# Kernel optimization log

Hardware: AMD Instinct MI355X
Metric: run time of the kernel (lower is better)

Reference implementation:

```python
import jax, jax.numpy as jnp
import numpy as np

B, T, C = 2, 2048, 2048
NH, NKVH = 16, 4
HS = C // NH          # 128
KV = NKVH * HS        # 512
ROPE_BASE = 10000.0


def setup_inputs() -> dict:
    key = jax.random.key(0)
    k0, k1, k2 = jax.random.split(key, 3)
    x = jax.random.normal(k0, (B, T, C), dtype=jnp.float32)
    w_qkv = jax.random.normal(k1, (C, C + 2 * KV), dtype=jnp.float32) * 0.02
    b_qkv = jnp.zeros((C + 2 * KV,), dtype=jnp.float32)
    w_proj = jax.random.normal(k2, (C, C), dtype=jnp.float32) * 0.02
    b_proj = jnp.zeros((C,), dtype=jnp.float32)
    # RoPE frequencies: freqs_cis[t, j] = exp(i * t * base^(-2j/HS)), j in [0, HS/2)
    inv_freq = 1.0 / (ROPE_BASE ** (jnp.arange(0, HS, 2, dtype=jnp.float32) / HS))
    ang = jnp.arange(T, dtype=jnp.float32)[:, None] * inv_freq[None, :]  # [T, HS/2]
    return {
        "x": x, "w_qkv": w_qkv, "b_qkv": b_qkv,
        "w_proj": w_proj, "b_proj": b_proj,
        "freqs_cos": jnp.cos(ang), "freqs_sin": jnp.sin(ang),
    }


def _apply_rope(x, cos, sin):
    # x: [B, T, H, HS]; pairs (even, odd) along last dim are (real, imag)
    b, t, h, d = x.shape
    x_ = x.reshape(b, t, h, d // 2, 2)
    xr, xi = x_[..., 0], x_[..., 1]
    cos = cos[None, :, None, :]  # [1, T, 1, HS/2]
    sin = sin[None, :, None, :]
    out_r = xr * cos - xi * sin
    out_i = xr * sin + xi * cos
    return jnp.stack([out_r, out_i], axis=-1).reshape(b, t, h, d)


def reference(x, w_qkv, b_qkv, w_proj, b_proj, freqs_cos, freqs_sin):
    qkv = x @ w_qkv + b_qkv                      # [B, T, C + 2*KV]
    q, k, v = jnp.split(qkv, [C, C + KV], axis=2)
    q = q.reshape(B, T, NH, HS)
    k = k.reshape(B, T, NKVH, HS)
    v = v.reshape(B, T, NKVH, HS).transpose(0, 2, 1, 3)  # [B, NKVH, T, HS]
    q = _apply_rope(q, freqs_cos, freqs_sin)
    k = _apply_rope(k, freqs_cos, freqs_sin)
    q = q.transpose(0, 2, 1, 3)                  # [B, NH, T, HS]
    k = k.transpose(0, 2, 1, 3)                  # [B, NKVH, T, HS]
    kv_cache = (k, v)
    rep = NH // NKVH
    k_full = jnp.repeat(k, rep, axis=1)          # repeat_interleave on head dim
    v_full = jnp.repeat(v, rep, axis=1)
    scores = jnp.einsum("bhqd,bhkd->bhqk", q, k_full) / jnp.sqrt(jnp.float32(HS))
    causal = jnp.tril(jnp.ones((T, T), dtype=bool))
    scores = jnp.where(causal[None, None], scores, jnp.finfo(scores.dtype).min)
    attn = jax.nn.softmax(scores, axis=-1)
    y = jnp.einsum("bhqk,bhkd->bhqd", attn, v_full)
    y = y.transpose(0, 2, 1, 3).reshape(B, T, C)
    y = y @ w_proj + b_proj
    return y, kv_cache[0], kv_cache[1]
```

## Files before the change

kernel.cpp:

```cpp
#include <hip/hip_runtime.h>

typedef unsigned short u16;
typedef unsigned int u32;

#define B_    2
#define T_    2048
#define C_    2048
#define NH_   16
#define NKVH_ 4
#define HS_   128
#define NQKV  3072
#define M_    4096
#define SCALE 0.08838834764831845f
#define CC    0.12751742f
#define THR_RAW 62.0f

typedef __bf16 bf16x8 __attribute__((ext_vector_type(8)));
typedef float  f32x4  __attribute__((ext_vector_type(4)));
typedef float  f32x16 __attribute__((ext_vector_type(16)));
typedef unsigned int u32x2 __attribute__((ext_vector_type(2)));

__device__ __forceinline__ float bf2f(u16 u) {
    union { u32 i; float f; } x; x.i = ((u32)u) << 16; return x.f;
}
__device__ __forceinline__ u16 f2bf(float f) {
    union { float f; u32 i; } x; x.f = f;
    u32 r = x.i + 0x7fffu + ((x.i >> 16) & 1u);
    return (u16)(r >> 16);
}
__device__ __forceinline__ u32 cvtpk(float lo, float hi) {
    u32 r; asm("v_cvt_pk_bf16_f32 %0, %1, %2" : "=v"(r) : "v"(lo), "v"(hi));
    return r;
}

__device__ __forceinline__ void gload16(const void* g, void* l) {
    __builtin_amdgcn_global_load_lds(
        (const __attribute__((address_space(1))) u32*)g,
        (__attribute__((address_space(3))) u32*)l,
        16, 0, 0);
}

__global__ __launch_bounds__(256) void cast_f32_bf16(
    const float* __restrict__ in, u16* __restrict__ out, int n)
{
    int idx = (blockIdx.x * 256 + threadIdx.x) * 4;
    if (idx < n) {
        float4 v = *reinterpret_cast<const float4*>(in + idx);
        u32 p0 = (u32)f2bf(v.x) | ((u32)f2bf(v.y) << 16);
        u32 p1 = (u32)f2bf(v.z) | ((u32)f2bf(v.w) << 16);
        u32* o = (u32*)(out + idx);
        o[0] = p0; o[1] = p1;
    }
}

__global__ __launch_bounds__(256) void transpose_cast_f32_bf16(
    const float* __restrict__ in, u16* __restrict__ out, int R, int Cc)
{
    __shared__ float tile[32][33];
    int c0 = blockIdx.x * 32, r0 = blockIdx.y * 32;
    int tx = threadIdx.x & 31, ty = threadIdx.x >> 5;
#pragma unroll
    for (int i = 0; i < 4; ++i)
        tile[ty + i * 8][tx] = in[(size_t)(r0 + ty + i * 8) * Cc + c0 + tx];
    __syncthreads();
#pragma unroll
    for (int i = 0; i < 4; ++i)
        out[(size_t)(c0 + ty + i * 8) * R + r0 + tx] = f2bf(tile[tx][ty + i * 8]);
}

__global__ __launch_bounds__(256) void transpose_bf16_batched(
    const u16* __restrict__ in, u16* __restrict__ out, int R, int Cc)
{
    __shared__ u16 tile[32][33];
    int c0 = blockIdx.x * 32, r0 = blockIdx.y * 32;
    size_t zb = (size_t)blockIdx.z * R * Cc;
    int tx = threadIdx.x & 31, ty = threadIdx.x >> 5;
#pragma unroll
    for (int i = 0; i < 4; ++i)
        tile[ty + i * 8][tx] = in[zb + (size_t)(r0 + ty + i * 8) * Cc + c0 + tx];
    __syncthreads();
#pragma unroll
    for (int i = 0; i < 4; ++i)
        out[zb + (size_t)(c0 + ty + i * 8) * R + r0 + tx] = tile[tx][ty + i * 8];
}

template <int MFRAG, int OUT_BF16>
__global__ __launch_bounds__(512, 2) void gemm8(
    const u16* __restrict__ A, const u16* __restrict__ Bt,
    const float* __restrict__ bias, void* __restrict__ Cv,
    int M, int N, int K)
{
    constexpr int MH = MFRAG / 2;
    constexpr int LA = MFRAG / 4;
    constexpr int ASZ = MFRAG * 1024;
    __shared__ __attribute__((aligned(16))) u16 As[2][2][ASZ];
    __shared__ __attribute__((aligned(16))) u16 Bs[2][2][8192];

    int tid = threadIdx.x, lane = tid & 63, w = tid >> 6;
    int l16 = lane & 15, hi = (lane >> 4) & 3;
    int wm = w >> 2, wn = w & 3;

    int gx = gridDim.x, nwg = gx * gridDim.y;
    int id = blockIdx.y * gx + blockIdx.x;
    int nid = (id & 7) * (nwg >> 3) + (id >> 3);
    int brow = (nid % gx) * (MFRAG * 32), bcol = (nid / gx) * 256;

    const int NT = K >> 6;
    f32x4 acc[MFRAG][4] = {};

    auto stageA = [&](int kt2, int kk, int buf) {
#pragma unroll
        for (int i = 0; i < LA; ++i) {
            u32 off = (u32)i * 8192 + (u32)w * 1024 + ((u32)lane << 4);
            u32 g = off ^ (((off >> 7) & 7) << 4);
            u32 r = g >> 6, s = (g >> 4) & 3;
            gload16(A + (size_t)(brow + r) * K + kt2 * 64 + kk * 32 + s * 8,
                    (char*)&As[buf][kk][0] + i * 8192 + w * 1024);
        }
    };
    auto stageB = [&](int kt2, int kk, int buf) {
#pragma unroll
        for (int i = 0; i < 2; ++i) {
            u32 off = (u32)i * 8192 + (u32)w * 1024 + ((u32)lane << 4);
            u32 g = off ^ (((off >> 7) & 7) << 4);
            u32 r = g >> 6, s = (g >> 4) & 3;
            gload16(Bt + (size_t)(bcol + r) * K + kt2 * 64 + kk * 32 + s * 8,
                    (char*)&Bs[buf][kk][0] + i * 8192 + w * 1024);
        }
    };
    auto readA = [&](const u16* base, int mh, bf16x8* dst) {
#pragma unroll
        for (int m = 0; m < MH; ++m) {
            u32 a = (u32)((wm * MFRAG + mh * MH + m) * 16 + l16) * 64 + (u32)hi * 16;
            dst[m] = *reinterpret_cast<const bf16x8*>(
                (const char*)base + (a ^ (((a >> 7) & 7) << 4)));
        }
    };
    auto readB = [&](const u16* base, bf16x8* dst) {
#pragma unroll
        for (int n = 0; n < 4; ++n) {
            u32 a = (u32)(wn * 64 + n * 16 + l16) * 64 + (u32)hi * 16;
            dst[n] = *reinterpret_cast<const bf16x8*>(
                (const char*)base + (a ^ (((a >> 7) & 7) << 4)));
        }
    };

    stageA(0, 0, 0); stageB(0, 0, 0); stageA(0, 1, 0); stageB(0, 1, 0);
    if (NT > 1) {
        stageA(1, 0, 1); stageB(1, 0, 1); stageA(1, 1, 1);
        if constexpr (MFRAG == 8) asm volatile("s_waitcnt vmcnt(6)" ::: "memory");
        else                      asm volatile("s_waitcnt vmcnt(4)" ::: "memory");
    } else {
        asm volatile("s_waitcnt vmcnt(0)" ::: "memory");
    }
    __builtin_amdgcn_s_barrier();

    for (int kt = 0; kt < NT; ++kt) {
        int cur = kt & 1, nxt = cur ^ 1;
        const u16* Ac0 = &As[cur][0][0];
        const u16* Ac1 = &As[cur][1][0];
        const u16* Bc0 = &Bs[cur][0][0];
        const u16* Bc1 = &Bs[cur][1][0];
        bf16x8 af0[MH], af1[MH], af2[MH], af3[MH], bf0[4], bf1[4];

        readA(Ac0, 0, af0); readB(Bc0, bf0); readA(Ac0, 1, af1);
        if (kt + 1 < NT) stageB(kt + 1, 1, nxt);
        __builtin_amdgcn_s_barrier();
        __builtin_amdgcn_s_setprio(1);
#pragma unroll
        for (int m = 0; m < MH; ++m)
#pragma unroll
            for (int n = 0; n < 4; ++n)
                acc[m][n] = __builtin_amdgcn_mfma_f32_16x16x32_bf16(
                    af0[m], bf0[n], acc[m][n], 0, 0, 0);
        __builtin_amdgcn_s_setprio(0);
        __builtin_amdgcn_s_barrier();

        readA(Ac1, 0, af2); readB(Bc1, bf1);
        if (kt + 2 < NT) stageA(kt + 2, 0, cur);
        __builtin_amdgcn_s_barrier();
        __builtin_amdgcn_s_setprio(1);
#pragma unroll
        for (int m = 0; m < MH; ++m)
#pragma unroll
            for (int n = 0; n < 4; ++n)
                acc[MH + m][n] = __builtin_amdgcn_mfma_f32_16x16x32_bf16(
                    af1[m], bf0[n], acc[MH + m][n], 0, 0, 0);
        __builtin_amdgcn_s_setprio(0);
        __builtin_amdgcn_s_barrier();

        readA(Ac1, 1, af3);
        if (kt + 2 < NT) stageB(kt + 2, 0, cur);
        __builtin_amdgcn_s_barrier();
        __builtin_amdgcn_s_setprio(1);
#pragma unroll
        for (int m = 0; m < MH; ++m)
#pragma unroll
            for (int n = 0; n < 4; ++n)
                acc[m][n] = __builtin_amdgcn_mfma_f32_16x16x32_bf16(
                    af2[m], bf1[n], acc[m][n], 0, 0, 0);
        __builtin_amdgcn_s_setprio(0);
        __builtin_amdgcn_s_barrier();

        if (kt + 2 < NT) stageA(kt + 2, 1, cur);
        __builtin_amdgcn_s_barrier();
        __builtin_amdgcn_s_setprio(1);
#pragma unroll
        for (int m = 0; m < MH; ++m)
#pragma unroll
            for (int n = 0; n < 4; ++n)
                acc[MH + m][n] = __builtin_amdgcn_mfma_f32_16x16x32_bf16(
                    af3[m], bf1[n], acc[MH + m][n], 0, 0, 0);
        __builtin_amdgcn_s_setprio(0);
        if (kt + 1 < NT) {
            if (kt + 2 < NT) {
                if constexpr (MFRAG == 8) asm volatile("s_waitcnt vmcnt(6)" ::: "memory");
                else                      asm volatile("s_waitcnt vmcnt(4)" ::: "memory");
            } else {
                asm volatile("s_waitcnt vmcnt(0)" ::: "memory");
            }
        }
        __builtin_amdgcn_s_barrier();
    }

#pragma unroll
    for (int n = 0; n < 4; ++n) {
        int col = bcol + wn * 64 + n * 16 + l16;
        float bv = bias[col];
#pragma unroll
        for (int m = 0; m < MFRAG; ++m) {
#pragma unroll
            for (int j = 0; j < 4; ++j) {
                int row = brow + wm * (MFRAG * 16) + m * 16 + hi * 4 + j;
                float v = acc[m][n][j] + bv;
                if (OUT_BF16)
                    ((u16*)Cv)[(size_t)row * N + col] = f2bf(v);
                else
                    ((float*)Cv)[(size_t)row * N + col] = v;
            }
        }
    }
}

__global__ __launch_bounds__(256) void rope_scatter(
    const u16* __restrict__ qkv,
    const float* __restrict__ fcos, const float* __restrict__ fsin,
    u16* __restrict__ qb, u16* __restrict__ kb, u16* __restrict__ vb,
    float* __restrict__ kc, float* __restrict__ vc)
{
    int bt = blockIdx.x;
    int b = bt >> 11, t = bt & 2047;
    const u16* row = qkv + (size_t)bt * NQKV;
    for (int s = threadIdx.x; s < NQKV / 2; s += 256) {
        int col = s * 2;
        if (col < C_) {
            int h = col >> 7, d = col & 127;
            float xr = bf2f(row[col]), xi = bf2f(row[col + 1]);
            int fi = t * 64 + (d >> 1);
            float c = fcos[fi], sn = fsin[fi];
            size_t o = ((size_t)(b * NH_ + h) * T_ + t) * HS_ + d;
            qb[o]     = f2bf(xr * c - xi * sn);
            qb[o + 1] = f2bf(xr * sn + xi * c);
        } else if (col < C_ + NKVH_ * HS_) {
            int cc = col - C_;
            int h = cc >> 7, d = cc & 127;
            float xr = bf2f(row[col]), xi = bf2f(row[col + 1]);
            int fi = t * 64 + (d >> 1);
            float c = fcos[fi], sn = fsin[fi];
            float yr = xr * c - xi * sn, yi = xr * sn + xi * c;
            size_t o = ((size_t)(b * NKVH_ + h) * T_ + t) * HS_ + d;
            kb[o] = f2bf(yr); kb[o + 1] = f2bf(yi);
            kc[o] = yr;       kc[o + 1] = yi;
        } else {
            int cc = col - (C_ + NKVH_ * HS_);
            int h = cc >> 7, d = cc & 127;
            float v0 = bf2f(row[col]), v1 = bf2f(row[col + 1]);
            size_t o = ((size_t)(b * NKVH_ + h) * T_ + t) * HS_ + d;
            vb[o] = f2bf(v0); vb[o + 1] = f2bf(v1);
            vc[o] = v0;       vc[o + 1] = v1;
        }
    }
}

#define STAGE_KV(it_, buf_)                                               \
  {                                                                       \
    int _it = (it_);                                                      \
    _Pragma("unroll")                                                     \
    for (int i = 0; i < 4; ++i) {                                         \
      int chunk = w * 4 + i;                                              \
      int rk = chunk * 4 + (lane >> 4);                                   \
      int ck = ((lane & 15) ^ (rk & 7)) << 3;                             \
      gload16(Kp + (size_t)(_it * 64 + rk) * HS_ + ck,                    \
              (char*)Ks[buf_] + chunk * 1024);                            \
      int rv = chunk * 8 + (lane >> 3);                                   \
      int cv = ((lane & 7) ^ (rv & 7)) << 3;                              \
      gload16(Vp + (size_t)rv * T_ + _it * 64 + cv,                       \
              (char*)Vs[buf_] + chunk * 1024);                            \
    }                                                                     \
  }

__global__ __launch_bounds__(256, 2) void attn_kernel(
    const u16* __restrict__ qb,
    const u16* __restrict__ kb,
    const u16* __restrict__ vt,
    u16* __restrict__ aout)
{
    __shared__ __attribute__((aligned(16))) u16 Ks[2][64 * 128];
    __shared__ __attribute__((aligned(16))) u16 Vs[2][128 * 64];

    int xx = blockIdx.x, yy = blockIdx.y;
    int qt = (yy < 16) ? (15 - xx) : xx;
    int bh = yy, b = bh >> 4, h = bh & 15, kvh = h >> 2;
    int lane = threadIdx.x & 63, w = threadIdx.x >> 6;
    int l32 = lane & 31, l5 = lane >> 5;
    int xorm = (l32 & 7) << 3;
    int koff = 8 * l5;

    const u16* Qp = qb + ((size_t)(b * NH_ + h) * T_ + qt * 128 + w * 32) * HS_;
    const u16* Kp = kb + (size_t)(b * NKVH_ + kvh) * T_ * HS_;
    const u16* Vp = vt + (size_t)(b * NKVH_ + kvh) * HS_ * T_;

    bf16x8 qf[8];
#pragma unroll
    for (int kd = 0; kd < 8; ++kd)
        qf[kd] = *reinterpret_cast<const bf16x8*>(
            Qp + (size_t)l32 * HS_ + kd * 16 + koff);

    f32x16 o[4] = {};
    float m = -1e30f, lrow = 0.f;
    int qg = qt * 128 + w * 32 + l32;
    int qmaxw = qt * 128 + w * 32 + 31;

    int ntiles = 2 * qt + 2;
    STAGE_KV(0, 0);

    for (int it = 0; it < ntiles; ++it) {
        int buf = it & 1;
        __syncthreads();
        if (it + 1 < ntiles) STAGE_KV(it + 1, buf ^ 1);

        if (it * 64 <= qmaxw) {
            const u16* Kbase = Ks[buf];
            const u16* Vbase = Vs[buf];

            f32x16 sacc[2] = {};
            __builtin_amdgcn_s_setprio(1);
#pragma unroll
            for (int kt2 = 0; kt2 < 2; ++kt2)
#pragma unroll
                for (int kd = 0; kd < 8; ++kd) {
                    bf16x8 kf = *reinterpret_cast<const bf16x8*>(
                        Kbase + (kt2 * 32 + l32) * 128 + ((kd * 16 + koff) ^ xorm));
                    sacc[kt2] = __builtin_amdgcn_mfma_f32_32x32x16_bf16(
                        kf, qf[kd], sacc[kt2], 0, 0, 0);
                }
            __builtin_amdgcn_s_setprio(0);

            if (it * 64 + 63 > qt * 128 + w * 32) {
#pragma unroll
                for (int kt2 = 0; kt2 < 2; ++kt2)
#pragma unroll
                    for (int r = 0; r < 16; ++r) {
                        int kvg = it * 64 + kt2 * 32 + (r & 3) + 8 * (r >> 2) + 4 * l5;
                        if (kvg > qg) sacc[kt2][r] = -1e30f;
                    }
            }

            float mx;
            {
                float t8[8];
#pragma unroll
                for (int i = 0; i < 8; ++i) {
                    float a = fmaxf(sacc[0][i], sacc[0][i + 8]);
                    float c = fmaxf(sacc[1][i], sacc[1][i + 8]);
                    t8[i] = fmaxf(a, c);
                }
                float t4a = fmaxf(t8[0], t8[1]), t4b = fmaxf(t8[2], t8[3]);
                float t4c = fmaxf(t8[4], t8[5]), t4d = fmaxf(t8[6], t8[7]);
                mx = fmaxf(fmaxf(t4a, t4b), fmaxf(t4c, t4d));
                mx = fmaxf(mx, __shfl_xor(mx, 32));
            }

            if (!__all(mx <= m + THR_RAW)) {
                float nm = fmaxf(m, mx);
                float al = exp2f(CC * (m - nm));
                m = nm;
                lrow *= al;
#pragma unroll
                for (int r = 0; r < 16; ++r) {
                    float af = __shfl(al, (r & 3) + 8 * (r >> 2) + 4 * l5, 64);
                    o[0][r] *= af; o[1][r] *= af; o[2][r] *= af; o[3][r] *= af;
                }
            }
            float mcm = -CC * m;

            f32x16 p[2];
#pragma unroll
            for (int kt2 = 0; kt2 < 2; ++kt2)
#pragma unroll
                for (int r = 0; r < 16; ++r)
                    p[kt2][r] = exp2f(__builtin_fmaf(CC, sacc[kt2][r], mcm));
            {
                float s8[8];
#pragma unroll
                for (int i = 0; i < 8; ++i)
                    s8[i] = (p[0][i] + p[0][i + 8]) + (p[1][i] + p[1][i + 8]);
                float s4a = s8[0] + s8[1], s4b = s8[2] + s8[3];
                float s4c = s8[4] + s8[5], s4d = s8[6] + s8[7];
                float rs = (s4a + s4b) + (s4c + s4d);
                rs += __shfl_xor(rs, 32);
                lrow += rs;
            }

            __builtin_amdgcn_s_setprio(1);
#pragma unroll
            for (int ks = 0; ks < 4; ++ks) {
                int e = ks & 1, kh = ks >> 1;
                u32 a0 = cvtpk(p[kh][8 * e + 0], p[kh][8 * e + 1]);
                u32 a1 = cvtpk(p[kh][8 * e + 2], p[kh][8 * e + 3]);
                u32 b0 = cvtpk(p[kh][8 * e + 4], p[kh][8 * e + 5]);
                u32 b1 = cvtpk(p[kh][8 * e + 6], p[kh][8 * e + 7]);
                u32x2 s0 = __builtin_amdgcn_permlane32_swap(a0, b0, false, false);
                u32x2 s1 = __builtin_amdgcn_permlane32_swap(a1, b1, false, false);
                union { u32 u[4]; bf16x8 v; } pu;
                pu.u[0] = s0[0]; pu.u[1] = s1[0]; pu.u[2] = s0[1]; pu.u[3] = s1[1];
                bf16x8 pf = pu.v;
#pragma unroll
                for (int dt = 0; dt < 4; ++dt) {
                    bf16x8 vf = *reinterpret_cast<const bf16x8*>(
                        Vbase + (dt * 32 + l32) * 64 + ((ks * 16 + koff) ^ xorm));
                    o[dt] = __builtin_amdgcn_mfma_f32_32x32x16_bf16(
                        pf, vf, o[dt], 0, 0, 0);
                }
            }
            __builtin_amdgcn_s_setprio(0);
        }
    }

    float inv = 1.0f / lrow;
#pragma unroll
    for (int r = 0; r < 16; ++r) {
        int ql = (r & 3) + 8 * (r >> 2) + 4 * l5;
        float iv = __shfl(inv, ql, 64);
        int trow = qt * 128 + w * 32 + ql;
        size_t base = ((size_t)b * T_ + trow) * C_ + h * HS_ + l32;
#pragma unroll
        for (int dt = 0; dt < 4; ++dt)
            aout[base + dt * 32] = f2bf(o[dt][r] * iv);
    }
}

extern "C" void kernel_launch(void* const* d_in, const int* in_sizes, int n_in,
                              void* d_out, int out_size, void* d_ws, size_t ws_size,
                              hipStream_t stream)
{
    const float* x      = (const float*)d_in[0];
    const float* w_qkv  = (const float*)d_in[1];
    const float* b_qkv  = (const float*)d_in[2];
    const float* w_proj = (const float*)d_in[3];
    const float* b_proj = (const float*)d_in[4];
    const float* fcos   = (const float*)d_in[5];
    const float* fsin   = (const float*)d_in[6];

    float* y  = (float*)d_out;
    float* kc = y + (size_t)B_ * T_ * C_;
    float* vc = kc + (size_t)B_ * NKVH_ * T_ * HS_;

    char* ws = (char*)d_ws;
    u16* xb     = (u16*)(ws);
    u16* wprojT = (u16*)(ws);
    u16* wqkvT = (u16*)(ws + 16777216);
    u16* kbuf  = (u16*)(ws + 16777216);
    u16* vbuf  = (u16*)(ws + 16777216 + 4194304);
    u16* vtb   = (u16*)(ws + 16777216 + 8388608);
    u16* qkv  = (u16*)(ws + 29360128);
    u16* aout = (u16*)(ws + 29360128);
    u16* qbuf = (u16*)(ws + 54525952);

    cast_f32_bf16<<<M_ * C_ / 1024, 256, 0, stream>>>(x, xb, M_ * C_);
    transpose_cast_f32_bf16<<<dim3(NQKV / 32, C_ / 32), 256, 0, stream>>>(
        w_qkv, wqkvT, C_, NQKV);
    gemm8<8, 1><<<dim3(M_ / 256, NQKV / 256), 512, 0, stream>>>(
        xb, wqkvT, b_qkv, qkv, M_, NQKV, C_);
    rope_scatter<<<M_, 256, 0, stream>>>(qkv, fcos, fsin, qbuf, kbuf, vbuf, kc, vc);
    transpose_bf16_batched<<<dim3(HS_ / 32, T_ / 32, B_ * NKVH_), 256, 0, stream>>>(
        vbuf, vtb, T_, HS_);
    transpose_cast_f32_bf16<<<dim3(C_ / 32, C_ / 32), 256, 0, stream>>>(
        w_proj, wprojT, C_, C_);
    attn_kernel<<<dim3(T_ / 128, B_ * NH_), 256, 0, stream>>>(qbuf, kbuf, vtb, aout);
    gemm8<4, 0><<<dim3(M_ / 128, C_ / 256), 512, 0, stream>>>(
        aout, wprojT, b_proj, y, M_, C_, C_);
}
```

Measured before the change: 233.6 us.

## Enlarge attention Q tile to 256 rows with 8 waves sharing KV tiles

The attention kernel now uses 512 threads per block and a 256-row query tile, so each staged K/V tile in shared memory serves eight waves and global KV traffic per query row drops. Each wave stages half as many chunks. The QK^T MFMA chain is split into two independent accumulators to shorten the dependency chain, and the s_setprio hints are removed. The reversed-order load-balancing tile mapping is dropped, leaving fewer, larger blocks with causal imbalance, and within a block the early waves idle at barriers while later ones work.

```diff
diff --git a/kernel.cpp b/kernel.cpp
--- a/kernel.cpp
+++ b/kernel.cpp
@@ -286,8 +286,8 @@
   {                                                                       \
     int _it = (it_);                                                      \
     _Pragma("unroll")                                                     \
-    for (int i = 0; i < 4; ++i) {                                         \
-      int chunk = w * 4 + i;                                              \
+    for (int i = 0; i < 2; ++i) {                                         \
+      int chunk = w * 2 + i;                                              \
       int rk = chunk * 4 + (lane >> 4);                                   \
       int ck = ((lane & 15) ^ (rk & 7)) << 3;                             \
       gload16(Kp + (size_t)(_it * 64 + rk) * HS_ + ck,                    \
@@ -299,7 +299,7 @@
     }                                                                     \
   }
 
-__global__ __launch_bounds__(256, 2) void attn_kernel(
+__global__ __launch_bounds__(512, 2) void attn_kernel(
     const u16* __restrict__ qb,
     const u16* __restrict__ kb,
     const u16* __restrict__ vt,
@@ -308,15 +308,14 @@
     __shared__ __attribute__((aligned(16))) u16 Ks[2][64 * 128];
     __shared__ __attribute__((aligned(16))) u16 Vs[2][128 * 64];
 
-    int xx = blockIdx.x, yy = blockIdx.y;
-    int qt = (yy < 16) ? (15 - xx) : xx;
-    int bh = yy, b = bh >> 4, h = bh & 15, kvh = h >> 2;
+    int qt = blockIdx.x;
+    int bh = blockIdx.y, b = bh >> 4, h = bh & 15, kvh = h >> 2;
     int lane = threadIdx.x & 63, w = threadIdx.x >> 6;
     int l32 = lane & 31, l5 = lane >> 5;
     int xorm = (l32 & 7) << 3;
     int koff = 8 * l5;
 
-    const u16* Qp = qb + ((size_t)(b * NH_ + h) * T_ + qt * 128 + w * 32) * HS_;
+    const u16* Qp = qb + ((size_t)(b * NH_ + h) * T_ + qt * 256 + w * 32) * HS_;
     const u16* Kp = kb + (size_t)(b * NKVH_ + kvh) * T_ * HS_;
     const u16* Vp = vt + (size_t)(b * NKVH_ + kvh) * HS_ * T_;
 
@@ -328,10 +327,11 @@
 
     f32x16 o[4] = {};
     float m = -1e30f, lrow = 0.f;
-    int qg = qt * 128 + w * 32 + l32;
-    int qmaxw = qt * 128 + w * 32 + 31;
-
-    int ntiles = 2 * qt + 2;
+    int rbase = qt * 256 + w * 32;
+    int qg = rbase + l32;
+    int qmaxw = rbase + 31;
+
+    int ntiles = 4 * qt + 4;
     STAGE_KV(0, 0);
 
     for (int it = 0; it < ntiles; ++it) {
@@ -343,20 +343,23 @@
             const u16* Kbase = Ks[buf];
             const u16* Vbase = Vs[buf];
 
-            f32x16 sacc[2] = {};
-            __builtin_amdgcn_s_setprio(1);
-#pragma unroll
-            for (int kt2 = 0; kt2 < 2; ++kt2)
-#pragma unroll
-                for (int kd = 0; kd < 8; ++kd) {
-                    bf16x8 kf = *reinterpret_cast<const bf16x8*>(
+            f32x16 sacc[2];
+#pragma unroll
+            for (int kt2 = 0; kt2 < 2; ++kt2) {
+                f32x16 slo = {}, shi = {};
+#pragma unroll
+                for (int kd = 0; kd < 4; ++kd) {
+                    bf16x8 kf0 = *reinterpret_cast<const bf16x8*>(
                         Kbase + (kt2 * 32 + l32) * 128 + ((kd * 16 + koff) ^ xorm));
-                    sacc[kt2] = __builtin_amdgcn_mfma_f32_32x32x16_bf16(
-                        kf, qf[kd], sacc[kt2], 0, 0, 0);
+                    bf16x8 kf1 = *reinterpret_cast<const bf16x8*>(
+                        Kbase + (kt2 * 32 + l32) * 128 + (((kd + 4) * 16 + koff) ^ xorm));
+                    slo = __builtin_amdgcn_mfma_f32_32x32x16_bf16(kf0, qf[kd], slo, 0, 0, 0);
+                    shi = __builtin_amdgcn_mfma_f32_32x32x16_bf16(kf1, qf[kd + 4], shi, 0, 0, 0);
                 }
-            __builtin_amdgcn_s_setprio(0);
-
-            if (it * 64 + 63 > qt * 128 + w * 32) {
+                sacc[kt2] = slo + shi;
+            }
+
+            if (it * 64 + 63 > rbase) {
 #pragma unroll
                 for (int kt2 = 0; kt2 < 2; ++kt2)
 #pragma unroll
@@ -412,7 +415,6 @@
                 lrow += rs;
             }
 
-            __builtin_amdgcn_s_setprio(1);
 #pragma unroll
             for (int ks = 0; ks < 4; ++ks) {
                 int e = ks & 1, kh = ks >> 1;
@@ -433,7 +435,6 @@
                         pf, vf, o[dt], 0, 0, 0);
                 }
             }
-            __builtin_amdgcn_s_setprio(0);
         }
     }
 
@@ -442,7 +443,7 @@
     for (int r = 0; r < 16; ++r) {
         int ql = (r & 3) + 8 * (r >> 2) + 4 * l5;
         float iv = __shfl(inv, ql, 64);
-        int trow = qt * 128 + w * 32 + ql;
+        int trow = rbase + ql;
         size_t base = ((size_t)b * T_ + trow) * C_ + h * HS_ + l32;
 #pragma unroll
         for (int dt = 0; dt < 4; ++dt)
@@ -487,7 +488,7 @@
         vbuf, vtb, T_, HS_);
     transpose_cast_f32_bf16<<<dim3(C_ / 32, C_ / 32), 256, 0, stream>>>(
         w_proj, wprojT, C_, C_);
-    attn_kernel<<<dim3(T_ / 128, B_ * NH_), 256, 0, stream>>>(qbuf, kbuf, vtb, aout);
+    attn_kernel<<<dim3(T_ / 256, B_ * NH_), 512, 0, stream>>>(qbuf, kbuf, vtb, aout);
     gemm8<4, 0><<<dim3(M_ / 128, C_ / 256), 512, 0, stream>>>(
         aout, wprojT, b_proj, y, M_, C_, C_);
 }
```

New measurement: 251.0 us. +7.4%, slower.

## Fuse RoPE and head scatter into QKV GEMM epilogue; drop attention setprio

Applied to the files above, without the earlier changes.

The QKV GEMM now applies RoPE directly in its epilogue. It pairs even and odd columns with a lane shuffle and writes q/k/v bf16 buffers plus the fp32 k/v cache outputs. This removes the separate rope_scatter kernel and the bf16 qkv intermediate round trip through memory. RoPE is now computed on fp32 accumulators rather than rounded bf16 values, and the epilogue does more scattered global stores and cos/sin loads per element. The workspace layout is reshuffled to match, and the s_setprio hints around the MFMA blocks in the attention kernel are removed, which changes wave scheduling priority.

```diff
diff --git a/kernel.cpp b/kernel.cpp
--- a/kernel.cpp
+++ b/kernel.cpp
@@ -9,6 +9,7 @@
 #define NH_   16
 #define NKVH_ 4
 #define HS_   128
+#define KV_   512
 #define NQKV  3072
 #define M_    4096
 #define SCALE 0.08838834764831845f
@@ -84,11 +85,14 @@
         out[zb + (size_t)(c0 + ty + i * 8) * R + r0 + tx] = tile[tx][ty + i * 8];
 }
 
-template <int MFRAG, int OUT_BF16>
+template <int MFRAG, int EPI>
 __global__ __launch_bounds__(512, 2) void gemm8(
     const u16* __restrict__ A, const u16* __restrict__ Bt,
     const float* __restrict__ bias, void* __restrict__ Cv,
-    int M, int N, int K)
+    int M, int N, int K,
+    const float* __restrict__ fcos, const float* __restrict__ fsin,
+    u16* __restrict__ qb, u16* __restrict__ kb, u16* __restrict__ vb,
+    float* __restrict__ kc, float* __restrict__ vc)
 {
     constexpr int MH = MFRAG / 2;
     constexpr int LA = MFRAG / 4;
@@ -223,61 +227,56 @@
         __builtin_amdgcn_s_barrier();
     }
 
-#pragma unroll
-    for (int n = 0; n < 4; ++n) {
-        int col = bcol + wn * 64 + n * 16 + l16;
-        float bv = bias[col];
-#pragma unroll
-        for (int m = 0; m < MFRAG; ++m) {
-#pragma unroll
-            for (int j = 0; j < 4; ++j) {
-                int row = brow + wm * (MFRAG * 16) + m * 16 + hi * 4 + j;
-                float v = acc[m][n][j] + bv;
-                if (OUT_BF16)
-                    ((u16*)Cv)[(size_t)row * N + col] = f2bf(v);
-                else
-                    ((float*)Cv)[(size_t)row * N + col] = v;
-            }
-        }
-    }
-}
-
-__global__ __launch_bounds__(256) void rope_scatter(
-    const u16* __restrict__ qkv,
-    const float* __restrict__ fcos, const float* __restrict__ fsin,
-    u16* __restrict__ qb, u16* __restrict__ kb, u16* __restrict__ vb,
-    float* __restrict__ kc, float* __restrict__ vc)
-{
-    int bt = blockIdx.x;
-    int b = bt >> 11, t = bt & 2047;
-    const u16* row = qkv + (size_t)bt * NQKV;
-    for (int s = threadIdx.x; s < NQKV / 2; s += 256) {
-        int col = s * 2;
-        if (col < C_) {
-            int h = col >> 7, d = col & 127;
-            float xr = bf2f(row[col]), xi = bf2f(row[col + 1]);
-            int fi = t * 64 + (d >> 1);
-            float c = fcos[fi], sn = fsin[fi];
-            size_t o = ((size_t)(b * NH_ + h) * T_ + t) * HS_ + d;
-            qb[o]     = f2bf(xr * c - xi * sn);
-            qb[o + 1] = f2bf(xr * sn + xi * c);
-        } else if (col < C_ + NKVH_ * HS_) {
-            int cc = col - C_;
-            int h = cc >> 7, d = cc & 127;
-            float xr = bf2f(row[col]), xi = bf2f(row[col + 1]);
-            int fi = t * 64 + (d >> 1);
-            float c = fcos[fi], sn = fsin[fi];
-            float yr = xr * c - xi * sn, yi = xr * sn + xi * c;
-            size_t o = ((size_t)(b * NKVH_ + h) * T_ + t) * HS_ + d;
-            kb[o] = f2bf(yr); kb[o + 1] = f2bf(yi);
-            kc[o] = yr;       kc[o + 1] = yi;
-        } else {
-            int cc = col - (C_ + NKVH_ * HS_);
-            int h = cc >> 7, d = cc & 127;
-            float v0 = bf2f(row[col]), v1 = bf2f(row[col + 1]);
-            size_t o = ((size_t)(b * NKVH_ + h) * T_ + t) * HS_ + d;
-            vb[o] = f2bf(v0); vb[o + 1] = f2bf(v1);
-            vc[o] = v0;       vc[o + 1] = v1;
+    if constexpr (EPI == 2) {
+        int sgn = l16 & 1;
+#pragma unroll
+        for (int n = 0; n < 4; ++n) {
+            int col = bcol + wn * 64 + n * 16 + l16;
+            float bv = bias[col];
+#pragma unroll
+            for (int m = 0; m < MFRAG; ++m) {
+#pragma unroll
+                for (int j = 0; j < 4; ++j) {
+                    int row = brow + wm * (MFRAG * 16) + m * 16 + hi * 4 + j;
+                    int bb = row >> 11, t = row & 2047;
+                    float v = acc[m][n][j] + bv;
+                    float pr = __shfl_xor(v, 1);
+                    if (col < C_) {
+                        int h = col >> 7, d = col & 127;
+                        float c = fcos[t * 64 + (d >> 1)];
+                        float s = fsin[t * 64 + (d >> 1)];
+                        float out = sgn ? (pr * s + v * c) : (v * c - pr * s);
+                        qb[((size_t)(bb * NH_ + h) * T_ + t) * HS_ + d] = f2bf(out);
+                    } else if (col < C_ + KV_) {
+                        int cc = col - C_;
+                        int h = cc >> 7, d = cc & 127;
+                        float c = fcos[t * 64 + (d >> 1)];
+                        float s = fsin[t * 64 + (d >> 1)];
+                        float out = sgn ? (pr * s + v * c) : (v * c - pr * s);
+                        size_t o = ((size_t)(bb * NKVH_ + h) * T_ + t) * HS_ + d;
+                        kb[o] = f2bf(out); kc[o] = out;
+                    } else {
+                        int cc = col - C_ - KV_;
+                        int h = cc >> 7, d = cc & 127;
+                        size_t o = ((size_t)(bb * NKVH_ + h) * T_ + t) * HS_ + d;
+                        vb[o] = f2bf(v); vc[o] = v;
+                    }
+                }
+            }
+        }
+    } else {
+#pragma unroll
+        for (int n = 0; n < 4; ++n) {
+            int col = bcol + wn * 64 + n * 16 + l16;
+            float bv = bias[col];
+#pragma unroll
+            for (int m = 0; m < MFRAG; ++m) {
+#pragma unroll
+                for (int j = 0; j < 4; ++j) {
+                    int row = brow + wm * (MFRAG * 16) + m * 16 + hi * 4 + j;
+                    ((float*)Cv)[(size_t)row * N + col] = acc[m][n][j] + bv;
+                }
+            }
         }
     }
 }
@@ -344,7 +343,6 @@
             const u16* Vbase = Vs[buf];
 
             f32x16 sacc[2] = {};
-            __builtin_amdgcn_s_setprio(1);
 #pragma unroll
             for (int kt2 = 0; kt2 < 2; ++kt2)
 #pragma unroll
@@ -354,7 +352,6 @@
                     sacc[kt2] = __builtin_amdgcn_mfma_f32_32x32x16_bf16(
                         kf, qf[kd], sacc[kt2], 0, 0, 0);
                 }
-            __builtin_amdgcn_s_setprio(0);
 
             if (it * 64 + 63 > qt * 128 + w * 32) {
 #pragma unroll
@@ -412,7 +409,6 @@
                 lrow += rs;
             }
 
-            __builtin_amdgcn_s_setprio(1);
 #pragma unroll
             for (int ks = 0; ks < 4; ++ks) {
                 int e = ks & 1, kh = ks >> 1;
@@ -433,7 +429,6 @@
                         pf, vf, o[dt], 0, 0, 0);
                 }
             }
-            __builtin_amdgcn_s_setprio(0);
         }
     }
 
@@ -469,25 +464,25 @@
     char* ws = (char*)d_ws;
     u16* xb     = (u16*)(ws);
     u16* wprojT = (u16*)(ws);
-    u16* wqkvT = (u16*)(ws + 16777216);
-    u16* kbuf  = (u16*)(ws + 16777216);
-    u16* vbuf  = (u16*)(ws + 16777216 + 4194304);
-    u16* vtb   = (u16*)(ws + 16777216 + 8388608);
-    u16* qkv  = (u16*)(ws + 29360128);
-    u16* aout = (u16*)(ws + 29360128);
-    u16* qbuf = (u16*)(ws + 54525952);
+    u16* vtb    = (u16*)(ws + 8388608);
+    u16* wqkvT  = (u16*)(ws + 16777216);
+    u16* aout   = (u16*)(ws + 16777216);
+    u16* qbuf   = (u16*)(ws + 33554432);
+    u16* kbuf   = (u16*)(ws + 50331648);
+    u16* vbuf   = (u16*)(ws + 54525952);
 
     cast_f32_bf16<<<M_ * C_ / 1024, 256, 0, stream>>>(x, xb, M_ * C_);
     transpose_cast_f32_bf16<<<dim3(NQKV / 32, C_ / 32), 256, 0, stream>>>(
         w_qkv, wqkvT, C_, NQKV);
-    gemm8<8, 1><<<dim3(M_ / 256, NQKV / 256), 512, 0, stream>>>(
-        xb, wqkvT, b_qkv, qkv, M_, NQKV, C_);
-    rope_scatter<<<M_, 256, 0, stream>>>(qkv, fcos, fsin, qbuf, kbuf, vbuf, kc, vc);
+    gemm8<8, 2><<<dim3(M_ / 256, NQKV / 256), 512, 0, stream>>>(
+        xb, wqkvT, b_qkv, nullptr, M_, NQKV, C_,
+        fcos, fsin, qbuf, kbuf, vbuf, kc, vc);
     transpose_bf16_batched<<<dim3(HS_ / 32, T_ / 32, B_ * NKVH_), 256, 0, stream>>>(
         vbuf, vtb, T_, HS_);
     transpose_cast_f32_bf16<<<dim3(C_ / 32, C_ / 32), 256, 0, stream>>>(
         w_proj, wprojT, C_, C_);
     attn_kernel<<<dim3(T_ / 128, B_ * NH_), 256, 0, stream>>>(qbuf, kbuf, vtb, aout);
     gemm8<4, 0><<<dim3(M_ / 128, C_ / 256), 512, 0, stream>>>(
-        aout, wprojT, b_proj, y, M_, C_, C_);
-}
+        aout, wprojT, b_proj, y, M_, C_, C_,
+        nullptr, nullptr, nullptr, nullptr, nullptr, nullptr, nullptr);
+}
```

Result: slower. 252.6 us (+8.1%).
